# Kernel optimization log

Measured on AMD Instinct MI355X. Metric: run time of the kernel, lower is better.

## Reference

```python
import jax, jax.numpy as jnp
import numpy as np

N_S = 50000
N_T = 50000
E = 800000
D_IN = 128
D_OUT = 128


def setup_inputs() -> dict:
    key = jax.random.key(0)
    k1, k2, k3, k4 = jax.random.split(key, 4)
    edge_index = jax.random.randint(k1, (2, E), 0, N_S, dtype=jnp.int64)
    x_s = jax.random.normal(k2, (N_S, D_IN), dtype=jnp.float32)
    x_t = jax.random.normal(k3, (N_T, D_IN), dtype=jnp.float32)
    # glorot-ish linear weight of GCNConv (bias=False)
    W = jax.random.normal(k4, (D_IN, D_OUT), dtype=jnp.float32) * (1.0 / np.sqrt(D_IN))
    return {"edge_index": edge_index, "x_s": x_s, "x_t": x_t, "W": W}


def reference(edge_index, x_s, x_t, W):
    N_s = x_s.shape[0]
    N_t = x_t.shape[0]
    N = N_s + N_t
    # dropout p=0.0 -> identity; concat bipartite features
    x = jnp.concatenate([x_s, x_t], axis=0)  # [N, d_in]
    row = edge_index[0]
    col = edge_index[1] + N_s  # module shifts target indices in-place
    # GCNConv: add self-loops with weight 1
    loops = jnp.arange(N, dtype=row.dtype)
    row_f = jnp.concatenate([row, loops])
    col_f = jnp.concatenate([col, loops])
    w = jnp.ones(row_f.shape[0], dtype=x.dtype)
    # symmetric degree normalization: deg computed on target (col)
    deg = jax.ops.segment_sum(w, col_f, num_segments=N)
    deg_inv_sqrt = jnp.where(deg > 0, jax.lax.rsqrt(deg), 0.0)
    norm = deg_inv_sqrt[row_f] * deg_inv_sqrt[col_f]  # [E+N]
    # linear transform then normalized scatter-add aggregation
    h = x @ W  # [N, d_out]
    msg = h[row_f] * norm[:, None]  # gather + scale, [E+N, d_out]
    out = jax.ops.segment_sum(msg, col_f, num_segments=N)  # scatter-add
    out = jax.nn.relu(out)
    return out[:N_s], out[N_s:]
```

## Files before the change

### kernel.cpp

```cpp
#include <hip/hip_runtime.h>
#include <hip/hip_bf16.h>
#include <math.h>

#define NSRC 50000
#define NTGT 50000
#define NTOT 100000
#define NEDGE 800000
#define DIM 128

#define NBUCK 782
#define BCAP 1536
#define BPAD 16
#define BLK 512
#define EPT 4
#define EPB2 2048
#define PBLK2 391
#define GEMM_GRID 782
#define FGRID 1173

typedef __attribute__((ext_vector_type(8))) short short8;
typedef __attribute__((ext_vector_type(4))) float float4v;

union U8 { short8 s; uint4 u; };

__device__ __forceinline__ unsigned short f2bf(float f) {
    unsigned u = __float_as_uint(f);
    unsigned r = (u + 0x7FFFu + ((u >> 16) & 1u)) >> 16;
    return (unsigned short)r;
}
__device__ __forceinline__ float bf2f(unsigned us) {
    return __uint_as_float(us << 16);
}
__device__ __forceinline__ unsigned pkbf(float lo, float hi) {
    __hip_bfloat162 b = __float22bfloat162_rn(make_float2(lo, hi));
    return *(unsigned*)&b;
}

__global__ __launch_bounds__(256) void k_prep(const float* __restrict__ W,
                                              unsigned short* __restrict__ Wt,
                                              int* __restrict__ bcnt) {
    int i = blockIdx.x * 256 + threadIdx.x;
    if (i < NBUCK * BPAD) bcnt[i] = 0;
    int j = i & 7, lane = (i >> 3) & 63, ts = i >> 9;
    int t = ts >> 2, s = ts & 3;
    int nl = lane & 15, qd = lane >> 4;
    Wt[i] = f2bf(W[(s * 32 + qd * 8 + j) * DIM + (t * 16 + nl)]);
}

__global__ __launch_bounds__(BLK) void k_front(const int* __restrict__ row,
                                               const int* __restrict__ col,
                                               int* __restrict__ bcnt,
                                               unsigned* __restrict__ part,
                                               const float* __restrict__ xsrc,
                                               const float* __restrict__ xtgt,
                                               const unsigned short* __restrict__ Wt,
                                               unsigned short* __restrict__ h,
                                               float* __restrict__ out) {
    __shared__ union SM {
        struct { int hist[NBUCK]; int runbase[NBUCK]; int cur[NBUCK]; } p;
        unsigned short Bs[DIM * DIM];
    } sm;

    const int tid = threadIdx.x;
    const int bid = blockIdx.x;

    if (bid % 3 == 0) {
        for (int i = tid; i < NBUCK; i += BLK) sm.p.hist[i] = 0;
        __syncthreads();

        int e0 = (bid / 3) * EPB2 + tid * EPT;
        bool valid = (e0 + EPT <= NEDGE);
        int c[EPT], r[EPT];
        if (valid) {
            *(int4*)&c[0] = *(const int4*)(col + e0);
            *(int4*)&r[0] = *(const int4*)(row + e0);
#pragma unroll
            for (int i = 0; i < EPT; ++i) atomicAdd(&sm.p.hist[c[i] >> 6], 1);
        }
        __syncthreads();
        for (int i = tid; i < NBUCK; i += BLK) {
            sm.p.runbase[i] = atomicAdd(&bcnt[i * BPAD], sm.p.hist[i]);
            sm.p.cur[i] = 0;
        }
        __syncthreads();
        if (valid) {
#pragma unroll
            for (int i = 0; i < EPT; ++i) {
                int q = c[i] >> 6;
                int pos = sm.p.runbase[q] + atomicAdd(&sm.p.cur[q], 1);
                part[q * BCAP + pos] = (unsigned)r[i] | ((unsigned)(c[i] & 63) << 16);
            }
        }
        return;
    }

    const int gb = bid - bid / 3 - 1;

    for (int idx = tid; idx < 2048; idx += BLK)
        ((uint4*)sm.Bs)[idx] = ((const uint4*)Wt)[idx];

    const int wave = tid >> 6, lane = tid & 63;
    const int nl = lane & 15, quad = lane >> 4;

    int node = gb * 128 + wave * 16 + nl;
    int mc = (node < NTOT) ? node : (NTOT - 1);
    const float* xrow = (mc < NSRC) ? (xsrc + (size_t)mc * DIM)
                                    : (xtgt + (size_t)(mc - NSRC) * DIM);
    float4 a[8];
#pragma unroll
    for (int s = 0; s < 4; ++s) {
        a[2 * s]     = *(const float4*)(xrow + s * 32 + quad * 8);
        a[2 * s + 1] = *(const float4*)(xrow + s * 32 + quad * 8 + 4);
    }
    __syncthreads();

    float4v acc[8];
#pragma unroll
    for (int t = 0; t < 8; ++t) acc[t] = (float4v){0.f, 0.f, 0.f, 0.f};

#pragma unroll
    for (int s = 0; s < 4; ++s) {
        U8 af;
        af.u.x = pkbf(a[2 * s].x, a[2 * s].y);
        af.u.y = pkbf(a[2 * s].z, a[2 * s].w);
        af.u.z = pkbf(a[2 * s + 1].x, a[2 * s + 1].y);
        af.u.w = pkbf(a[2 * s + 1].z, a[2 * s + 1].w);
#pragma unroll
        for (int t = 0; t < 8; ++t) {
            short8 bf = *(const short8*)&sm.Bs[((t * 4 + s) * 64 + lane) * 8];
            acc[t] = __builtin_amdgcn_mfma_f32_16x16x32_bf16(bf, af.s, acc[t], 0, 0, 0);
        }
    }

    if (node < NTOT) {
        unsigned short* hp = h + (size_t)node * DIM + quad * 4;
        float* op = out + (size_t)node * DIM + quad * 4;
        bool isrc = (node < NSRC);
#pragma unroll
        for (int t = 0; t < 8; ++t) {
            uint2 p;
            p.x = pkbf(acc[t][0], acc[t][1]);
            p.y = pkbf(acc[t][2], acc[t][3]);
            *(uint2*)(hp + t * 16) = p;
            if (isrc) {
                float4 o;
                o.x = fmaxf(acc[t][0], 0.f);
                o.y = fmaxf(acc[t][1], 0.f);
                o.z = fmaxf(acc[t][2], 0.f);
                o.w = fmaxf(acc[t][3], 0.f);
                *(float4*)(op + t * 16) = o;
            }
        }
    }
}

__global__ __launch_bounds__(BLK) void k_back(const int* __restrict__ bcnt,
                                              const unsigned* __restrict__ part,
                                              const unsigned short* __restrict__ h,
                                              float* __restrict__ out) {
    __shared__ unsigned ebuf[BCAP];
    __shared__ unsigned short srt[BCAP];
    __shared__ int hist[64], bufA[64], bufB[64], cur[64], st[64];

    int q = blockIdx.x, tid = threadIdx.x;
    int n = bcnt[q * BPAD];
    int base = q * BCAP;

    if (tid < 64) hist[tid] = 0;
    __syncthreads();
    for (int i = tid; i < n; i += BLK) {
        unsigned p = part[base + i];
        ebuf[i] = p;
        atomicAdd(&hist[p >> 16], 1);
    }
    __syncthreads();

    if (tid < 64) bufA[tid] = hist[tid];
    int* src = bufA; int* dst = bufB;
    for (int d = 1; d < 64; d <<= 1) {
        __syncthreads();
        if (tid < 64) dst[tid] = src[tid] + ((tid >= d) ? src[tid - d] : 0);
        int* tp = src; src = dst; dst = tp;
    }
    __syncthreads();
    if (tid < 64) {
        int excl = src[tid] - hist[tid];
        cur[tid] = excl;
        st[tid] = excl;
    }
    __syncthreads();
    for (int i = tid; i < n; i += BLK) {
        unsigned p = ebuf[i];
        int pos = atomicAdd(&cur[p >> 16], 1);
        srt[pos] = (unsigned short)(p & 0xffffu);
    }
    __syncthreads();

    int w = tid >> 6, lane = tid & 63;
    int qd = lane >> 4, ql = lane & 15;

    for (int t = 0; t < 8; ++t) {
        int cl = w * 8 + t;
        int c = q * 64 + cl;
        if (c >= NTGT) break;
        int nn = hist[cl];
        int s0 = st[cl];

        float acc[8];
#pragma unroll
        for (int i = 0; i < 8; ++i) acc[i] = 0.f;

        int kk = 0;
#pragma unroll 4
        for (; kk + 4 <= nn; kk += 4) {
            int r = (int)srt[s0 + kk + qd];
            uint4 d = *(const uint4*)(h + (size_t)r * DIM + ql * 8);
            acc[0] += bf2f(d.x & 0xffff); acc[1] += bf2f(d.x >> 16);
            acc[2] += bf2f(d.y & 0xffff); acc[3] += bf2f(d.y >> 16);
            acc[4] += bf2f(d.z & 0xffff); acc[5] += bf2f(d.z >> 16);
            acc[6] += bf2f(d.w & 0xffff); acc[7] += bf2f(d.w >> 16);
        }
        if (qd < nn - kk) {
            int r = (int)srt[s0 + kk + qd];
            uint4 d = *(const uint4*)(h + (size_t)r * DIM + ql * 8);
            acc[0] += bf2f(d.x & 0xffff); acc[1] += bf2f(d.x >> 16);
            acc[2] += bf2f(d.y & 0xffff); acc[3] += bf2f(d.y >> 16);
            acc[4] += bf2f(d.z & 0xffff); acc[5] += bf2f(d.z >> 16);
            acc[6] += bf2f(d.w & 0xffff); acc[7] += bf2f(d.w >> 16);
        }

#pragma unroll
        for (int i = 0; i < 8; ++i) {
            acc[i] += __shfl_xor(acc[i], 16, 64);
            acc[i] += __shfl_xor(acc[i], 32, 64);
        }

        if (qd == 0) {
            float di = rsqrtf(1.0f + (float)nn);
            float dd = di * di;
            uint4 dh = *(const uint4*)(h + (size_t)(NSRC + c) * DIM + ql * 8);
            float4 o0, o1;
            o0.x = fmaxf(di * acc[0] + dd * bf2f(dh.x & 0xffff), 0.f);
            o0.y = fmaxf(di * acc[1] + dd * bf2f(dh.x >> 16), 0.f);
            o0.z = fmaxf(di * acc[2] + dd * bf2f(dh.y & 0xffff), 0.f);
            o0.w = fmaxf(di * acc[3] + dd * bf2f(dh.y >> 16), 0.f);
            o1.x = fmaxf(di * acc[4] + dd * bf2f(dh.z & 0xffff), 0.f);
            o1.y = fmaxf(di * acc[5] + dd * bf2f(dh.z >> 16), 0.f);
            o1.z = fmaxf(di * acc[6] + dd * bf2f(dh.w & 0xffff), 0.f);
            o1.w = fmaxf(di * acc[7] + dd * bf2f(dh.w >> 16), 0.f);
            float* op = out + (size_t)(NSRC + c) * DIM + ql * 8;
            *(float4*)op = o0;
            *(float4*)(op + 4) = o1;
        }
    }
}

extern "C" void kernel_launch(void* const* d_in, const int* in_sizes, int n_in,
                              void* d_out, int out_size, void* d_ws, size_t ws_size,
                              hipStream_t stream) {
    const int* ei     = (const int*)d_in[0];
    const float* xsrc = (const float*)d_in[1];
    const float* xtgt = (const float*)d_in[2];
    const float* W    = (const float*)d_in[3];
    float* out = (float*)d_out;

    const int* row = ei;
    const int* col = ei + NEDGE;

    char* ws = (char*)d_ws;
    unsigned short* h  = (unsigned short*)ws;  ws += (size_t)NTOT * DIM * 2;
    unsigned short* Wt = (unsigned short*)ws;  ws += DIM * DIM * 2;
    unsigned* part = (unsigned*)ws;            ws += (size_t)NBUCK * BCAP * 4;
    int* bcnt = (int*)ws;                      ws += NBUCK * BPAD * 4;

    k_prep<<<64, 256, 0, stream>>>(W, Wt, bcnt);
    k_front<<<FGRID, BLK, 0, stream>>>(row, col, bcnt, part, xsrc, xtgt, Wt, h, out);
    k_back<<<NBUCK, BLK, 0, stream>>>(bcnt, part, h, out);
}
```

Measured before the change: 163.9 us.

## Split fused front kernel and reorder gather by source-row quarter

Splits the combined partition/GEMM kernel back into separate k_part and k_gemm launches. In k_back, edges are sorted by (source row >> 14, target column), so each wave walks all its 8 targets within one source-range quarter before moving to the next. This improves L2 locality of the gathered h rows. It costs 64 accumulator registers per lane, a larger 256-entry scan, a second read of part from global memory instead of LDS, and an extra kernel launch.

```diff
diff --git a/kernel.cpp b/kernel.cpp
--- a/kernel.cpp
+++ b/kernel.cpp
@@ -13,10 +13,9 @@
 #define BPAD 16
 #define BLK 512
 #define EPT 4
-#define EPB2 2048
-#define PBLK2 391
+#define EPB 2048
+#define PBLK 391
 #define GEMM_GRID 782
-#define FGRID 1173
 
 typedef __attribute__((ext_vector_type(8))) short short8;
 typedef __attribute__((ext_vector_type(4))) float float4v;
@@ -47,62 +46,55 @@
     Wt[i] = f2bf(W[(s * 32 + qd * 8 + j) * DIM + (t * 16 + nl)]);
 }
 
-__global__ __launch_bounds__(BLK) void k_front(const int* __restrict__ row,
-                                               const int* __restrict__ col,
-                                               int* __restrict__ bcnt,
-                                               unsigned* __restrict__ part,
-                                               const float* __restrict__ xsrc,
-                                               const float* __restrict__ xtgt,
-                                               const unsigned short* __restrict__ Wt,
-                                               unsigned short* __restrict__ h,
-                                               float* __restrict__ out) {
-    __shared__ union SM {
-        struct { int hist[NBUCK]; int runbase[NBUCK]; int cur[NBUCK]; } p;
-        unsigned short Bs[DIM * DIM];
-    } sm;
+__global__ __launch_bounds__(BLK) void k_part(const int* __restrict__ row,
+                                              const int* __restrict__ col,
+                                              int* __restrict__ bcnt,
+                                              unsigned* __restrict__ part) {
+    __shared__ int hist[NBUCK], runbase[NBUCK], cur[NBUCK];
+    int tid = threadIdx.x;
+    for (int i = tid; i < NBUCK; i += BLK) hist[i] = 0;
+    __syncthreads();
+
+    int e0 = blockIdx.x * EPB + tid * EPT;
+    bool valid = (e0 + EPT <= NEDGE);
+    int c[EPT], r[EPT];
+    if (valid) {
+        *(int4*)&c[0] = *(const int4*)(col + e0);
+        *(int4*)&r[0] = *(const int4*)(row + e0);
+#pragma unroll
+        for (int i = 0; i < EPT; ++i) atomicAdd(&hist[c[i] >> 6], 1);
+    }
+    __syncthreads();
+    for (int i = tid; i < NBUCK; i += BLK) {
+        runbase[i] = atomicAdd(&bcnt[i * BPAD], hist[i]);
+        cur[i] = 0;
+    }
+    __syncthreads();
+    if (valid) {
+#pragma unroll
+        for (int i = 0; i < EPT; ++i) {
+            int q = c[i] >> 6;
+            int pos = runbase[q] + atomicAdd(&cur[q], 1);
+            part[q * BCAP + pos] = (unsigned)r[i] | ((unsigned)(c[i] & 63) << 16);
+        }
+    }
+}
+
+__global__ __launch_bounds__(BLK) void k_gemm(const float* __restrict__ xsrc,
+                                              const float* __restrict__ xtgt,
+                                              const unsigned short* __restrict__ Wt,
+                                              unsigned short* __restrict__ h,
+                                              float* __restrict__ out) {
+    __shared__ unsigned short Bs[DIM * DIM];
 
     const int tid = threadIdx.x;
-    const int bid = blockIdx.x;
-
-    if (bid % 3 == 0) {
-        for (int i = tid; i < NBUCK; i += BLK) sm.p.hist[i] = 0;
-        __syncthreads();
-
-        int e0 = (bid / 3) * EPB2 + tid * EPT;
-        bool valid = (e0 + EPT <= NEDGE);
-        int c[EPT], r[EPT];
-        if (valid) {
-            *(int4*)&c[0] = *(const int4*)(col + e0);
-            *(int4*)&r[0] = *(const int4*)(row + e0);
-#pragma unroll
-            for (int i = 0; i < EPT; ++i) atomicAdd(&sm.p.hist[c[i] >> 6], 1);
-        }
-        __syncthreads();
-        for (int i = tid; i < NBUCK; i += BLK) {
-            sm.p.runbase[i] = atomicAdd(&bcnt[i * BPAD], sm.p.hist[i]);
-            sm.p.cur[i] = 0;
-        }
-        __syncthreads();
-        if (valid) {
-#pragma unroll
-            for (int i = 0; i < EPT; ++i) {
-                int q = c[i] >> 6;
-                int pos = sm.p.runbase[q] + atomicAdd(&sm.p.cur[q], 1);
-                part[q * BCAP + pos] = (unsigned)r[i] | ((unsigned)(c[i] & 63) << 16);
-            }
-        }
-        return;
-    }
-
-    const int gb = bid - bid / 3 - 1;
-
     for (int idx = tid; idx < 2048; idx += BLK)
-        ((uint4*)sm.Bs)[idx] = ((const uint4*)Wt)[idx];
+        ((uint4*)Bs)[idx] = ((const uint4*)Wt)[idx];
 
     const int wave = tid >> 6, lane = tid & 63;
     const int nl = lane & 15, quad = lane >> 4;
 
-    int node = gb * 128 + wave * 16 + nl;
+    int node = blockIdx.x * 128 + wave * 16 + nl;
     int mc = (node < NTOT) ? node : (NTOT - 1);
     const float* xrow = (mc < NSRC) ? (xsrc + (size_t)mc * DIM)
                                     : (xtgt + (size_t)(mc - NSRC) * DIM);
@@ -127,7 +119,7 @@
         af.u.w = pkbf(a[2 * s + 1].z, a[2 * s + 1].w);
 #pragma unroll
         for (int t = 0; t < 8; ++t) {
-            short8 bf = *(const short8*)&sm.Bs[((t * 4 + s) * 64 + lane) * 8];
+            short8 bf = *(const short8*)&Bs[((t * 4 + s) * 64 + lane) * 8];
             acc[t] = __builtin_amdgcn_mfma_f32_16x16x32_bf16(bf, af.s, acc[t], 0, 0, 0);
         }
     }
@@ -158,96 +150,100 @@
                                               const unsigned* __restrict__ part,
                                               const unsigned short* __restrict__ h,
                                               float* __restrict__ out) {
-    __shared__ unsigned ebuf[BCAP];
     __shared__ unsigned short srt[BCAP];
-    __shared__ int hist[64], bufA[64], bufB[64], cur[64], st[64];
+    __shared__ int hist[256], st[256], cur[256], bufA[256], bufB[256];
+    __shared__ int degs[64];
 
     int q = blockIdx.x, tid = threadIdx.x;
     int n = bcnt[q * BPAD];
     int base = q * BCAP;
 
-    if (tid < 64) hist[tid] = 0;
+    if (tid < 256) hist[tid] = 0;
     __syncthreads();
     for (int i = tid; i < n; i += BLK) {
         unsigned p = part[base + i];
-        ebuf[i] = p;
-        atomicAdd(&hist[p >> 16], 1);
-    }
-    __syncthreads();
-
-    if (tid < 64) bufA[tid] = hist[tid];
+        int key = (((p >> 14) & 3) << 6) | (p >> 16);
+        atomicAdd(&hist[key], 1);
+    }
+    __syncthreads();
+    if (tid < 64)
+        degs[tid] = hist[tid] + hist[tid + 64] + hist[tid + 128] + hist[tid + 192];
+    if (tid < 256) bufA[tid] = hist[tid];
     int* src = bufA; int* dst = bufB;
-    for (int d = 1; d < 64; d <<= 1) {
+    for (int d = 1; d < 256; d <<= 1) {
         __syncthreads();
-        if (tid < 64) dst[tid] = src[tid] + ((tid >= d) ? src[tid - d] : 0);
+        if (tid < 256) dst[tid] = src[tid] + ((tid >= d) ? src[tid - d] : 0);
         int* tp = src; src = dst; dst = tp;
     }
     __syncthreads();
-    if (tid < 64) {
-        int excl = src[tid] - hist[tid];
-        cur[tid] = excl;
-        st[tid] = excl;
-    }
+    if (tid < 256) { int e = src[tid] - hist[tid]; st[tid] = e; cur[tid] = e; }
     __syncthreads();
     for (int i = tid; i < n; i += BLK) {
-        unsigned p = ebuf[i];
-        int pos = atomicAdd(&cur[p >> 16], 1);
+        unsigned p = part[base + i];
+        int key = (((p >> 14) & 3) << 6) | (p >> 16);
+        int pos = atomicAdd(&cur[key], 1);
         srt[pos] = (unsigned short)(p & 0xffffu);
     }
     __syncthreads();
 
     int w = tid >> 6, lane = tid & 63;
     int qd = lane >> 4, ql = lane & 15;
-
+    int cl0 = w * 8;
+
+    float acc[8][8];
+#pragma unroll
+    for (int t = 0; t < 8; ++t)
+#pragma unroll
+        for (int j = 0; j < 8; ++j) acc[t][j] = 0.f;
+
+#pragma unroll
+    for (int p = 0; p < 4; ++p) {
+#pragma unroll
+        for (int t = 0; t < 8; ++t) {
+            int seg = (p << 6) | (cl0 + t);
+            int ns = hist[seg], s0 = st[seg];
+            int kk = 0;
+            for (; kk + 4 <= ns; kk += 4) {
+                int r = (int)srt[s0 + kk + qd];
+                uint4 d = *(const uint4*)(h + (size_t)r * DIM + ql * 8);
+                acc[t][0] += bf2f(d.x & 0xffff); acc[t][1] += bf2f(d.x >> 16);
+                acc[t][2] += bf2f(d.y & 0xffff); acc[t][3] += bf2f(d.y >> 16);
+                acc[t][4] += bf2f(d.z & 0xffff); acc[t][5] += bf2f(d.z >> 16);
+                acc[t][6] += bf2f(d.w & 0xffff); acc[t][7] += bf2f(d.w >> 16);
+            }
+            if (qd < ns - kk) {
+                int r = (int)srt[s0 + kk + qd];
+                uint4 d = *(const uint4*)(h + (size_t)r * DIM + ql * 8);
+                acc[t][0] += bf2f(d.x & 0xffff); acc[t][1] += bf2f(d.x >> 16);
+                acc[t][2] += bf2f(d.y & 0xffff); acc[t][3] += bf2f(d.y >> 16);
+                acc[t][4] += bf2f(d.z & 0xffff); acc[t][5] += bf2f(d.z >> 16);
+                acc[t][6] += bf2f(d.w & 0xffff); acc[t][7] += bf2f(d.w >> 16);
+            }
+        }
+    }
+
+#pragma unroll
     for (int t = 0; t < 8; ++t) {
-        int cl = w * 8 + t;
-        int c = q * 64 + cl;
-        if (c >= NTGT) break;
-        int nn = hist[cl];
-        int s0 = st[cl];
-
-        float acc[8];
-#pragma unroll
-        for (int i = 0; i < 8; ++i) acc[i] = 0.f;
-
-        int kk = 0;
-#pragma unroll 4
-        for (; kk + 4 <= nn; kk += 4) {
-            int r = (int)srt[s0 + kk + qd];
-            uint4 d = *(const uint4*)(h + (size_t)r * DIM + ql * 8);
-            acc[0] += bf2f(d.x & 0xffff); acc[1] += bf2f(d.x >> 16);
-            acc[2] += bf2f(d.y & 0xffff); acc[3] += bf2f(d.y >> 16);
-            acc[4] += bf2f(d.z & 0xffff); acc[5] += bf2f(d.z >> 16);
-            acc[6] += bf2f(d.w & 0xffff); acc[7] += bf2f(d.w >> 16);
-        }
-        if (qd < nn - kk) {
-            int r = (int)srt[s0 + kk + qd];
-            uint4 d = *(const uint4*)(h + (size_t)r * DIM + ql * 8);
-            acc[0] += bf2f(d.x & 0xffff); acc[1] += bf2f(d.x >> 16);
-            acc[2] += bf2f(d.y & 0xffff); acc[3] += bf2f(d.y >> 16);
-            acc[4] += bf2f(d.z & 0xffff); acc[5] += bf2f(d.z >> 16);
-            acc[6] += bf2f(d.w & 0xffff); acc[7] += bf2f(d.w >> 16);
-        }
-
-#pragma unroll
-        for (int i = 0; i < 8; ++i) {
-            acc[i] += __shfl_xor(acc[i], 16, 64);
-            acc[i] += __shfl_xor(acc[i], 32, 64);
-        }
-
-        if (qd == 0) {
+#pragma unroll
+        for (int j = 0; j < 8; ++j) {
+            acc[t][j] += __shfl_xor(acc[t][j], 16, 64);
+            acc[t][j] += __shfl_xor(acc[t][j], 32, 64);
+        }
+        int c = q * 64 + cl0 + t;
+        if (qd == 0 && c < NTGT) {
+            int nn = degs[cl0 + t];
             float di = rsqrtf(1.0f + (float)nn);
             float dd = di * di;
             uint4 dh = *(const uint4*)(h + (size_t)(NSRC + c) * DIM + ql * 8);
             float4 o0, o1;
-            o0.x = fmaxf(di * acc[0] + dd * bf2f(dh.x & 0xffff), 0.f);
-            o0.y = fmaxf(di * acc[1] + dd * bf2f(dh.x >> 16), 0.f);
-            o0.z = fmaxf(di * acc[2] + dd * bf2f(dh.y & 0xffff), 0.f);
-            o0.w = fmaxf(di * acc[3] + dd * bf2f(dh.y >> 16), 0.f);
-            o1.x = fmaxf(di * acc[4] + dd * bf2f(dh.z & 0xffff), 0.f);
-            o1.y = fmaxf(di * acc[5] + dd * bf2f(dh.z >> 16), 0.f);
-            o1.z = fmaxf(di * acc[6] + dd * bf2f(dh.w & 0xffff), 0.f);
-            o1.w = fmaxf(di * acc[7] + dd * bf2f(dh.w >> 16), 0.f);
+            o0.x = fmaxf(di * acc[t][0] + dd * bf2f(dh.x & 0xffff), 0.f);
+            o0.y = fmaxf(di * acc[t][1] + dd * bf2f(dh.x >> 16), 0.f);
+            o0.z = fmaxf(di * acc[t][2] + dd * bf2f(dh.y & 0xffff), 0.f);
+            o0.w = fmaxf(di * acc[t][3] + dd * bf2f(dh.y >> 16), 0.f);
+            o1.x = fmaxf(di * acc[t][4] + dd * bf2f(dh.z & 0xffff), 0.f);
+            o1.y = fmaxf(di * acc[t][5] + dd * bf2f(dh.z >> 16), 0.f);
+            o1.z = fmaxf(di * acc[t][6] + dd * bf2f(dh.w & 0xffff), 0.f);
+            o1.w = fmaxf(di * acc[t][7] + dd * bf2f(dh.w >> 16), 0.f);
             float* op = out + (size_t)(NSRC + c) * DIM + ql * 8;
             *(float4*)op = o0;
             *(float4*)(op + 4) = o1;
@@ -274,6 +270,7 @@
     int* bcnt = (int*)ws;                      ws += NBUCK * BPAD * 4;
 
     k_prep<<<64, 256, 0, stream>>>(W, Wt, bcnt);
-    k_front<<<FGRID, BLK, 0, stream>>>(row, col, bcnt, part, xsrc, xtgt, Wt, h, out);
+    k_part<<<PBLK, BLK, 0, stream>>>(row, col, bcnt, part);
+    k_gemm<<<GEMM_GRID, BLK, 0, stream>>>(xsrc, xtgt, Wt, h, out);
     k_back<<<NBUCK, BLK, 0, stream>>>(bcnt, part, h, out);
 }
```

New measurement: 197.0 us. 1.2x slower.

## Batch four target nodes per gather loop and coarsen edge partition blocks

Applied to the files above, without the earlier changes.

The aggregation kernel now handles four target nodes at once per wave, with independent accumulators, so more gather loads are in flight and memory latency is better hidden. Nodes with unequal degrees share one loop bounded by the largest degree, so some lanes sit idle behind per-node predicates. Separately, the partition stage uses 16 edges per thread in 98 leading blocks instead of interleaving small partition blocks with the GEMM blocks. That cuts global atomics on the bucket counters but reduces overlap between partitioning and the GEMM.

```diff
diff --git a/kernel.cpp b/kernel.cpp
--- a/kernel.cpp
+++ b/kernel.cpp
@@ -12,11 +12,11 @@
 #define BCAP 1536
 #define BPAD 16
 #define BLK 512
-#define EPT 4
-#define EPB2 2048
-#define PBLK2 391
+#define EPT 16
+#define EPB 8192
+#define PBLK 98
 #define GEMM_GRID 782
-#define FGRID 1173
+#define FGRID (PBLK + GEMM_GRID)
 
 typedef __attribute__((ext_vector_type(8))) short short8;
 typedef __attribute__((ext_vector_type(4))) float float4v;
@@ -64,16 +64,19 @@
     const int tid = threadIdx.x;
     const int bid = blockIdx.x;
 
-    if (bid % 3 == 0) {
+    if (bid < PBLK) {
         for (int i = tid; i < NBUCK; i += BLK) sm.p.hist[i] = 0;
         __syncthreads();
 
-        int e0 = (bid / 3) * EPB2 + tid * EPT;
+        int e0 = bid * EPB + tid * EPT;
         bool valid = (e0 + EPT <= NEDGE);
         int c[EPT], r[EPT];
         if (valid) {
-            *(int4*)&c[0] = *(const int4*)(col + e0);
-            *(int4*)&r[0] = *(const int4*)(row + e0);
+#pragma unroll
+            for (int v = 0; v < 4; ++v) {
+                *(int4*)&c[4 * v] = *(const int4*)(col + e0 + 4 * v);
+                *(int4*)&r[4 * v] = *(const int4*)(row + e0 + 4 * v);
+            }
 #pragma unroll
             for (int i = 0; i < EPT; ++i) atomicAdd(&sm.p.hist[c[i] >> 6], 1);
         }
@@ -94,7 +97,7 @@
         return;
     }
 
-    const int gb = bid - bid / 3 - 1;
+    const int gb = bid - PBLK;
 
     for (int idx = tid; idx < 2048; idx += BLK)
         ((uint4*)sm.Bs)[idx] = ((const uint4*)Wt)[idx];
@@ -198,61 +201,77 @@
 
     int w = tid >> 6, lane = tid & 63;
     int qd = lane >> 4, ql = lane & 15;
-
-    for (int t = 0; t < 8; ++t) {
-        int cl = w * 8 + t;
-        int c = q * 64 + cl;
-        if (c >= NTGT) break;
-        int nn = hist[cl];
-        int s0 = st[cl];
-
-        float acc[8];
-#pragma unroll
-        for (int i = 0; i < 8; ++i) acc[i] = 0.f;
-
-        int kk = 0;
-#pragma unroll 4
-        for (; kk + 4 <= nn; kk += 4) {
-            int r = (int)srt[s0 + kk + qd];
-            uint4 d = *(const uint4*)(h + (size_t)r * DIM + ql * 8);
-            acc[0] += bf2f(d.x & 0xffff); acc[1] += bf2f(d.x >> 16);
-            acc[2] += bf2f(d.y & 0xffff); acc[3] += bf2f(d.y >> 16);
-            acc[4] += bf2f(d.z & 0xffff); acc[5] += bf2f(d.z >> 16);
-            acc[6] += bf2f(d.w & 0xffff); acc[7] += bf2f(d.w >> 16);
-        }
-        if (qd < nn - kk) {
-            int r = (int)srt[s0 + kk + qd];
-            uint4 d = *(const uint4*)(h + (size_t)r * DIM + ql * 8);
-            acc[0] += bf2f(d.x & 0xffff); acc[1] += bf2f(d.x >> 16);
-            acc[2] += bf2f(d.y & 0xffff); acc[3] += bf2f(d.y >> 16);
-            acc[4] += bf2f(d.z & 0xffff); acc[5] += bf2f(d.z >> 16);
-            acc[6] += bf2f(d.w & 0xffff); acc[7] += bf2f(d.w >> 16);
-        }
-
+    int cl0 = w * 8;
+
+#define GATHER(ACC, NN, SS)                                                   \
+    if (e < NN) {                                                             \
+        int r = (int)srt[SS + e];                                             \
+        uint4 d = *(const uint4*)(h + (size_t)r * DIM + ql * 8);              \
+        ACC[0] += bf2f(d.x & 0xffff); ACC[1] += bf2f(d.x >> 16);              \
+        ACC[2] += bf2f(d.y & 0xffff); ACC[3] += bf2f(d.y >> 16);              \
+        ACC[4] += bf2f(d.z & 0xffff); ACC[5] += bf2f(d.z >> 16);              \
+        ACC[6] += bf2f(d.w & 0xffff); ACC[7] += bf2f(d.w >> 16);              \
+    }
+
+#define WRITEOUT(ACC, NN, CL)                                                 \
+    {                                                                         \
+        _Pragma("unroll")                                                     \
+        for (int i = 0; i < 8; ++i) {                                         \
+            ACC[i] += __shfl_xor(ACC[i], 16, 64);                             \
+            ACC[i] += __shfl_xor(ACC[i], 32, 64);                             \
+        }                                                                     \
+        int cgl = q * 64 + (CL);                                              \
+        if (qd == 0 && cgl < NTGT) {                                          \
+            float di = rsqrtf(1.0f + (float)NN);                              \
+            float dd = di * di;                                               \
+            uint4 dh = *(const uint4*)(h + (size_t)(NSRC + cgl) * DIM + ql * 8); \
+            float4 o0, o1;                                                    \
+            o0.x = fmaxf(di * ACC[0] + dd * bf2f(dh.x & 0xffff), 0.f);        \
+            o0.y = fmaxf(di * ACC[1] + dd * bf2f(dh.x >> 16), 0.f);           \
+            o0.z = fmaxf(di * ACC[2] + dd * bf2f(dh.y & 0xffff), 0.f);        \
+            o0.w = fmaxf(di * ACC[3] + dd * bf2f(dh.y >> 16), 0.f);           \
+            o1.x = fmaxf(di * ACC[4] + dd * bf2f(dh.z & 0xffff), 0.f);        \
+            o1.y = fmaxf(di * ACC[5] + dd * bf2f(dh.z >> 16), 0.f);           \
+            o1.z = fmaxf(di * ACC[6] + dd * bf2f(dh.w & 0xffff), 0.f);        \
+            o1.w = fmaxf(di * ACC[7] + dd * bf2f(dh.w >> 16), 0.f);           \
+            float* op = out + (size_t)(NSRC + cgl) * DIM + ql * 8;            \
+            *(float4*)op = o0;                                                \
+            *(float4*)(op + 4) = o1;                                          \
+        }                                                                     \
+    }
+
+    for (int g = 0; g < 2; ++g) {
+        int c0 = cl0 + g * 4;
+        int nA = hist[c0],     sA = st[c0];
+        int nB = hist[c0 + 1], sB = st[c0 + 1];
+        int nC = hist[c0 + 2], sC = st[c0 + 2];
+        int nD = hist[c0 + 3], sD = st[c0 + 3];
+
+        float accA[8], accB[8], accC[8], accD[8];
 #pragma unroll
         for (int i = 0; i < 8; ++i) {
-            acc[i] += __shfl_xor(acc[i], 16, 64);
-            acc[i] += __shfl_xor(acc[i], 32, 64);
-        }
-
-        if (qd == 0) {
-            float di = rsqrtf(1.0f + (float)nn);
-            float dd = di * di;
-            uint4 dh = *(const uint4*)(h + (size_t)(NSRC + c) * DIM + ql * 8);
-            float4 o0, o1;
-            o0.x = fmaxf(di * acc[0] + dd * bf2f(dh.x & 0xffff), 0.f);
-            o0.y = fmaxf(di * acc[1] + dd * bf2f(dh.x >> 16), 0.f);
-            o0.z = fmaxf(di * acc[2] + dd * bf2f(dh.y & 0xffff), 0.f);
-            o0.w = fmaxf(di * acc[3] + dd * bf2f(dh.y >> 16), 0.f);
-            o1.x = fmaxf(di * acc[4] + dd * bf2f(dh.z & 0xffff), 0.f);
-            o1.y = fmaxf(di * acc[5] + dd * bf2f(dh.z >> 16), 0.f);
-            o1.z = fmaxf(di * acc[6] + dd * bf2f(dh.w & 0xffff), 0.f);
-            o1.w = fmaxf(di * acc[7] + dd * bf2f(dh.w >> 16), 0.f);
-            float* op = out + (size_t)(NSRC + c) * DIM + ql * 8;
-            *(float4*)op = o0;
-            *(float4*)(op + 4) = o1;
-        }
-    }
+            accA[i] = 0.f; accB[i] = 0.f; accC[i] = 0.f; accD[i] = 0.f;
+        }
+
+        int m1 = (nA > nB) ? nA : nB;
+        int m2 = (nC > nD) ? nC : nD;
+        int mx = (m1 > m2) ? m1 : m2;
+        int itn = (mx + 3) >> 2;
+        for (int k = 0; k < itn; ++k) {
+            int e = 4 * k + qd;
+            GATHER(accA, nA, sA)
+            GATHER(accB, nB, sB)
+            GATHER(accC, nC, sC)
+            GATHER(accD, nD, sD)
+        }
+
+        WRITEOUT(accA, nA, c0)
+        WRITEOUT(accB, nB, c0 + 1)
+        WRITEOUT(accC, nC, c0 + 2)
+        WRITEOUT(accD, nD, c0 + 3)
+    }
+#undef GATHER
+#undef WRITEOUT
 }
 
 extern "C" void kernel_launch(void* const* d_in, const int* in_sizes, int n_in,
```

Result: faster. 158.8 us, median of 2 (-3.1%).
